# Performance work log

Hardware: AMD Instinct MI355X
Metric: run time of the kernel (lower is better)

## Reference

```python
import jax, jax.numpy as jnp
import numpy as np
import math

# ---- constants lifted verbatim from the torch source ----
PMLX = 10; PX = 400; TX = PMLX + PX + PMLX          # txsize = 420
PMLY = 10; PY = 400; TY = PMLY + PY + PMLY          # tysize = 420
CX = TX // 2; CY = TY // 2
EPS0 = 1e-9 / 36 / math.pi
MU0 = 4 * math.pi * 1e-7
C0 = 1.0 / math.sqrt(MU0 * EPS0)
DX = 2.5e-8; DY = 2.5e-8
DT = 0.99 / C0 / math.sqrt((1.0 / DX) ** 2 + (1.0 / DY) ** 2)
EPSR_INF = 5.283
EPS_INF = EPS0 * EPSR_INF
F0 = 5.47e14; BW = 0.1 * F0
T = math.sqrt(2.0) * math.sqrt(math.log(2.0)) / (math.pi * BW)
NSTEPS = 200   # reduced from 16000 for the correctness baseline; same per-step math


def setup_inputs() -> dict:
    # Lorentz (complex-pole) silver model from param(): pole/residue -> a0,a1,b0,b1,b2
    pr, pi_ = -4.8113e12, 6.8512e13
    rr, ri = 4.9581e14, -1.511e18
    a0 = -2.0 * (pr * rr + pi_ * ri)
    a1 = 2.0 * rr
    b0 = pr * pr + pi_ * pi_
    b1 = -2.0 * pr
    b2 = 1.0
    den = b0 * DT * DT + 2 * b1 * DT + 4 * b2
    Ca = np.array([-(2 * b0 * DT * DT - 8 * b2) / den], np.float32)
    Cb = np.array([-(b0 * DT * DT - 2 * b1 * DT + 4 * b2) / den], np.float32)
    Cc = np.array([(2 * a0 * EPS0 * DT + 4 * a1 * EPS0) / den], np.float32)
    Cd = np.array([-(8 * a1 * EPS0) / den], np.float32)
    Ce = np.array([(-2 * a0 * EPS0 * DT + 4 * a1 * EPS0) / den], np.float32)
    temp1 = float(Cc[0])                       # sum over tot_pol = 1 pole
    denom = EPS_INF / DT + 0.5 * temp1
    C1 = np.full((TX + 1, TY + 1), (EPS_INF / DT) / denom, np.float32)
    C2 = np.full((TX + 1, TY + 1), 0.5 / denom, np.float32)
    Cb_dx = np.full((TX + 1, TY + 1), 1.0 / denom / DX, np.float32)
    Cb_dy = np.full((TX + 1, TY + 1), 1.0 / denom / DY, np.float32)
    dbhx = np.full((TX + 1, TY), DT / MU0 / DY, np.float32)   # Hx curl coeff
    dbhy = np.full((TX, TY + 1), DT / MU0 / DX, np.float32)   # Hy curl coeff
    # polynomial-graded PML conductivity profiles (pml_param)
    m = 4
    eta0 = 120.0 * math.pi
    smax = 0.8 * (m + 1) / (eta0 * DX)

    def prof(n, npml, off):
        k = np.arange(n, dtype=np.float64)
        dl = np.clip(npml - k - off, 0.0, None) / npml   # depth into left PML
        dr = np.clip(k + off - (n - 1 - npml), 0.0, None) / npml
        return (smax * (dl ** m + dr ** m)).astype(np.float32)

    sig_ex = prof(TX + 1, PMLX, 0.0)
    sig_ey = prof(TY + 1, PMLY, 0.0)
    sig_hx = prof(TX, PMLX, 0.5)   # H nodes on half-grid
    sig_hy = prof(TY, PMLY, 0.5)
    # Gaussian-modulated sine soft source at the grid center
    t = np.arange(NSTEPS, dtype=np.float64) * DT
    src = (np.exp(-(((t - 4 * T) / T) ** 2)) * np.sin(2 * math.pi * F0 * (t - 4 * T))).astype(np.float32)
    return {
        "src": jnp.asarray(src), "C1": jnp.asarray(C1), "C2": jnp.asarray(C2),
        "Cb_dx": jnp.asarray(Cb_dx), "Cb_dy": jnp.asarray(Cb_dy),
        "dbhx": jnp.asarray(dbhx), "dbhy": jnp.asarray(dbhy),
        "Ca": jnp.asarray(Ca), "Cb": jnp.asarray(Cb), "Cc": jnp.asarray(Cc),
        "Cd": jnp.asarray(Cd), "Ce": jnp.asarray(Ce),
        "sig_ex": jnp.asarray(sig_ex), "sig_ey": jnp.asarray(sig_ey),
        "sig_hx": jnp.asarray(sig_hx), "sig_hy": jnp.asarray(sig_hy),
        "n_steps": NSTEPS,
    }


def reference(src, C1, C2, Cb_dx, Cb_dy, dbhx, dbhy, Ca, Cb, Cc, Cd, Ce,
              sig_ex, sig_ey, sig_hx, sig_hy, n_steps):
    # PML damping factors (exponential time-stepping of the conductive loss)
    de = jnp.exp(-(sig_ex[:, None] + sig_ey[None, :]) * (DT / EPS0))     # (421,421) for Ez
    dhx = jnp.exp(-(sig_ex[:, None] + sig_hy[None, :]) * (DT / MU0))     # (421,420) for Hx
    dhy = jnp.exp(-(sig_hx[:, None] + sig_ey[None, :]) * (DT / MU0))     # (420,421) for Hy
    # PEC outer boundary mask
    mask = jnp.pad(jnp.ones((TX - 1, TY - 1), de.dtype), ((1, 1), (1, 1)))
    ca = Ca[:, None, None]; cb = Cb[:, None, None]; cc = Cc[:, None, None]
    cd = Cd[:, None, None]; ce = Ce[:, None, None]

    def step(carry, s):
        Ez, Eold, Hx, Hy, Jz, Jold = carry
        # H-field Yee updates with PML damping
        Hx = dhx * (Hx - dbhx * (Ez[:, 1:] - Ez[:, :-1]))
        Hy = dhy * (Hy + dbhy * (Ez[1:, :] - Ez[:-1, :]))
        # curls onto Ez nodes (interior), zero-padded at PEC boundary
        curlHy = jnp.pad(Hy[1:, :] - Hy[:-1, :], ((1, 1), (0, 0)))       # (421,421)
        curlHx = jnp.pad(Hx[:, 1:] - Hx[:, :-1], ((0, 0), (1, 1)))       # (421,421)
        # Lorentz ADE dispersion source term (tot_pol summed; Cc*Ez^{n+1} folded into C1/C2/Cb_*)
        Phi = jnp.sum((ca + 1.0) * Jz + cb * Jold + cd * Ez[None] + ce * Eold[None], axis=0)
        Ez_new = mask * de * (C1 * Ez + Cb_dx * curlHy - Cb_dy * curlHx - C2 * Phi)
        Ez_new = Ez_new.at[CX, CY].add(s)                                 # soft point source
        # polarization current recurrence
        Jz_new = ca * Jz + cb * Jold + cc * Ez_new[None] + cd * Ez[None] + ce * Eold[None]
        return (Ez_new, Ez, Hx, Hy, Jz_new, Jz), None

    z = jnp.zeros((TX + 1, TY + 1), src.dtype)
    init = (z, z,
            jnp.zeros((TX + 1, TY), src.dtype),
            jnp.zeros((TX, TY + 1), src.dtype),
            jnp.zeros((1, TX + 1, TY + 1), src.dtype),
            jnp.zeros((1, TX + 1, TY + 1), src.dtype))
    (Ez, _, _, _, _, _), _ = jax.lax.scan(step, init, src[:n_steps])
    return Ez
```

## Files before the change

### kernel.cpp

```cpp
#include <hip/hip_runtime.h>
#include <math.h>

#define NXr 421
#define CXr 210
#define NSTEPS_C 200

#define Bt   16
#define Kt   8
#define EXT  32
#define LROWS (EXT + 2)
#define SPITCH 36
#define NBLK 27
#define NPHASE (NSTEPS_C / Kt)

#define PP   448
#define PAD  8
#define CP   (CXr + PAD)
#define FSZ  (PP * PP)

struct PParams {
    float *aEz, *aEo, *aJz, *aJo, *aHx, *aHy;
    float *bEz, *bEo, *bJz, *bJo, *bHx, *bHy;
    const float *dexP, *deyP, *aexP, *aeyP, *ahxP, *ahyP;
    const float *C1a, *C2a, *Cbdxa, *Cbdya;
    const float *Caa, *Cba, *Cca, *Cda, *Cea, *dbhxa, *dbhya;
    const float *src;
};

__global__ void init_kernel(const float* __restrict__ sig_ex,
                            const float* __restrict__ sig_ey,
                            const float* __restrict__ sig_hx,
                            const float* __restrict__ sig_hy,
                            float de_fac, float dh_fac,
                            float* __restrict__ zero_base, int n_zero,
                            float* __restrict__ dexP, float* __restrict__ deyP,
                            float* __restrict__ aexP, float* __restrict__ aeyP,
                            float* __restrict__ ahxP, float* __restrict__ ahyP)
{
    int t = blockIdx.x * blockDim.x + threadIdx.x;
    int stride = gridDim.x * blockDim.x;
    for (int k = t; k < n_zero; k += stride) zero_base[k] = 0.0f;
    if (t < PP) {
        int g = t - PAD;
        dexP[t] = (g >= 1 && g <= NXr - 2) ? expf(-sig_ex[g] * de_fac) : 0.0f;
        deyP[t] = (g >= 1 && g <= NXr - 2) ? expf(-sig_ey[g] * de_fac) : 0.0f;
        aexP[t] = (g >= 0 && g <  NXr)     ? expf(-sig_ex[g] * dh_fac) : 0.0f;
        aeyP[t] = (g >= 0 && g <  NXr)     ? expf(-sig_ey[g] * dh_fac) : 0.0f;
        ahxP[t] = (g >= 0 && g <  NXr - 1) ? expf(-sig_hx[g] * dh_fac) : 0.0f;
        ahyP[t] = (g >= 0 && g <  NXr - 1) ? expf(-sig_hy[g] * dh_fac) : 0.0f;
    }
}

__global__ __launch_bounds__(256)
void phase_kernel(PParams p, int t, int b0, float* __restrict__ out,
                  int writeOut)
{
    __shared__ __align__(16) float sEz[2][LROWS][SPITCH];

    const int tid = threadIdx.x;
    const int tj = tid & 15, ti = tid >> 4;
    const int li0 = 2 * ti, lj0 = 2 * tj;

    const int gx = (int)gridDim.x;
    int orig = (int)blockIdx.y * gx + (int)blockIdx.x;
    int nwg = gx * gx;
    int q = nwg >> 3, rr = nwg & 7;
    int xcd = orig & 7, k = orig >> 3;
    int nid = (xcd < rr ? xcd * (q + 1) : rr * (q + 1) + (xcd - rr) * q) + k;
    int bx = nid % gx, by = nid / gx;

    const int r0 = (bx + b0) * Bt + li0;
    const int c0 = (by + b0) * Bt + lj0;

    const float ca = p.Caa[0], cb = p.Cba[0], cc = p.Cca[0];
    const float cd = p.Cda[0], ce = p.Cea[0];
    const float ca1 = ca + 1.0f;
    const float C1 = p.C1a[0], C2 = p.C2a[0];
    const float cbdx = p.Cbdxa[0], cbdy = p.Cbdya[0];
    const float dbhx0 = p.dbhxa[0], dbhy0 = p.dbhya[0];

    float dHx[2][2], dHy[2][2], dE[2][2], dHyU[2], dHxL[2];
    float srcw[2][2];
#pragma unroll
    for (int a = 0; a < 2; ++a)
#pragma unroll
        for (int b = 0; b < 2; ++b) {
            dHx[a][b] = p.aexP[r0 + a] * p.ahyP[c0 + b];
            dHy[a][b] = p.ahxP[r0 + a] * p.aeyP[c0 + b];
            dE[a][b]  = p.dexP[r0 + a] * p.deyP[c0 + b];
            srcw[a][b] = ((r0 + a == CP) && (c0 + b == CP)) ? 1.0f : 0.0f;
        }
    {
        float ahxU = (r0 > 0) ? p.ahxP[r0 - 1] : 0.0f;
        float ahyL = (c0 > 0) ? p.ahyP[c0 - 1] : 0.0f;
        dHyU[0] = ahxU * p.aeyP[c0];
        dHyU[1] = ahxU * p.aeyP[c0 + 1];
        dHxL[0] = p.aexP[r0] * ahyL;
        dHxL[1] = p.aexP[r0 + 1] * ahyL;
    }

    const bool odd = (t & 1) != 0;
    const float* cEz = odd ? p.bEz : p.aEz;
    const float* cEo = odd ? p.bEo : p.aEo;
    const float* cJz = odd ? p.bJz : p.aJz;
    const float* cJo = odd ? p.bJo : p.aJo;
    const float* cHx = odd ? p.bHx : p.aHx;
    const float* cHy = odd ? p.bHy : p.aHy;
    float* nEz = odd ? p.aEz : p.bEz;
    float* nEo = odd ? p.aEo : p.bEo;
    float* nJz = odd ? p.aJz : p.bJz;
    float* nJo = odd ? p.aJo : p.bJo;
    float* nHx = odd ? p.aHx : p.bHx;
    float* nHy = odd ? p.aHy : p.bHy;

    {
        float* sp = &sEz[0][0][0];
        for (int z = tid; z < 2 * LROWS * SPITCH; z += 256) sp[z] = 0.0f;
    }

    float ez[2][2], eo[2][2], jz[2][2], jo[2][2], hx[2][2], hy[2][2];
#pragma unroll
    for (int a = 0; a < 2; ++a) {
        int g = (r0 + a) * PP + c0;
        float2 v;
        v = *(const float2*)&cEz[g]; ez[a][0] = v.x; ez[a][1] = v.y;
        v = *(const float2*)&cEo[g]; eo[a][0] = v.x; eo[a][1] = v.y;
        v = *(const float2*)&cJz[g]; jz[a][0] = v.x; jz[a][1] = v.y;
        v = *(const float2*)&cJo[g]; jo[a][0] = v.x; jo[a][1] = v.y;
        v = *(const float2*)&cHx[g]; hx[a][0] = v.x; hx[a][1] = v.y;
        v = *(const float2*)&cHy[g]; hy[a][0] = v.x; hy[a][1] = v.y;
    }
    float hyU[2], hxL[2];
    {
        float2 v = *(const float2*)&cHy[(r0 - 1) * PP + c0];
        hyU[0] = v.x; hyU[1] = v.y;
        hxL[0] = cHx[r0 * PP + c0 - 1];
        hxL[1] = cHx[(r0 + 1) * PP + c0 - 1];
    }

    const int n0 = t * Kt;
    float svl[Kt];
#pragma unroll
    for (int s = 0; s < Kt; ++s) svl[s] = p.src[n0 + s];

    __syncthreads();

    for (int s = 0; s < Kt; ++s) {
        float (*S)[SPITCH] = sEz[s & 1];
        *(float2*)&S[1 + li0][2 + lj0] = make_float2(ez[0][0], ez[0][1]);
        *(float2*)&S[2 + li0][2 + lj0] = make_float2(ez[1][0], ez[1][1]);

        hx[0][0] = dHx[0][0] * (hx[0][0] - dbhx0 * (ez[0][1] - ez[0][0]));
        hx[1][0] = dHx[1][0] * (hx[1][0] - dbhx0 * (ez[1][1] - ez[1][0]));
        hy[0][0] = dHy[0][0] * (hy[0][0] + dbhy0 * (ez[1][0] - ez[0][0]));
        hy[0][1] = dHy[0][1] * (hy[0][1] + dbhy0 * (ez[1][1] - ez[0][1]));

        __syncthreads();

        float eR0 = S[1 + li0][4 + lj0];
        float eR1 = S[2 + li0][4 + lj0];
        float2 eD = *(float2*)&S[3 + li0][2 + lj0];
        float2 eU = *(float2*)&S[li0][2 + lj0];
        float eL0 = S[1 + li0][1 + lj0];
        float eL1 = S[2 + li0][1 + lj0];

        hx[0][1] = dHx[0][1] * (hx[0][1] - dbhx0 * (eR0 - ez[0][1]));
        hx[1][1] = dHx[1][1] * (hx[1][1] - dbhx0 * (eR1 - ez[1][1]));
        hy[1][0] = dHy[1][0] * (hy[1][0] + dbhy0 * (eD.x - ez[1][0]));
        hy[1][1] = dHy[1][1] * (hy[1][1] + dbhy0 * (eD.y - ez[1][1]));

        hyU[0] = dHyU[0] * (hyU[0] + dbhy0 * (ez[0][0] - eU.x));
        hyU[1] = dHyU[1] * (hyU[1] + dbhy0 * (ez[0][1] - eU.y));
        hxL[0] = dHxL[0] * (hxL[0] - dbhx0 * (ez[0][0] - eL0));
        hxL[1] = dHxL[1] * (hxL[1] - dbhx0 * (ez[1][0] - eL1));

        float sv = svl[s];
        float cHyv[2][2], cHxv[2][2];
        cHyv[0][0] = hy[0][0] - hyU[0];   cHxv[0][0] = hx[0][0] - hxL[0];
        cHyv[0][1] = hy[0][1] - hyU[1];   cHxv[0][1] = hx[0][1] - hx[0][0];
        cHyv[1][0] = hy[1][0] - hy[0][0]; cHxv[1][0] = hx[1][0] - hxL[1];
        cHyv[1][1] = hy[1][1] - hy[0][1]; cHxv[1][1] = hx[1][1] - hx[1][0];

#pragma unroll
        for (int a = 0; a < 2; ++a)
#pragma unroll
            for (int b = 0; b < 2; ++b) {
                float e = ez[a][b], eold = eo[a][b];
                float j = jz[a][b], jold = jo[a][b];
                float phi = ca1 * j + cb * jold + cd * e + ce * eold;
                float en = dE[a][b] *
                    (C1 * e + cbdx * cHyv[a][b] - cbdy * cHxv[a][b] - C2 * phi);
                en = fmaf(srcw[a][b], sv, en);
                float jn = phi - j + cc * en;
                eo[a][b] = e;  ez[a][b] = en;
                jo[a][b] = j;  jz[a][b] = jn;
            }
    }

    if (ti >= 4 && ti < 12 && tj >= 4 && tj < 12) {
#pragma unroll
        for (int a = 0; a < 2; ++a) {
            int g = (r0 + a) * PP + c0;
            *(float2*)&nEz[g] = make_float2(ez[a][0], ez[a][1]);
            *(float2*)&nEo[g] = make_float2(eo[a][0], eo[a][1]);
            *(float2*)&nJz[g] = make_float2(jz[a][0], jz[a][1]);
            *(float2*)&nJo[g] = make_float2(jo[a][0], jo[a][1]);
            *(float2*)&nHx[g] = make_float2(hx[a][0], hx[a][1]);
            *(float2*)&nHy[g] = make_float2(hy[a][0], hy[a][1]);
        }
        if (writeOut) {
#pragma unroll
            for (int a = 0; a < 2; ++a)
#pragma unroll
                for (int b = 0; b < 2; ++b) {
                    int gi = r0 + a - PAD, gj = c0 + b - PAD;
                    if (gi < NXr && gj < NXr)
                        out[gi * NXr + gj] = ez[a][b];
                }
        }
    }
}

extern "C" void kernel_launch(void* const* d_in, const int* in_sizes, int n_in,
                              void* d_out, int out_size, void* d_ws, size_t ws_size,
                              hipStream_t stream)
{
    const float* src    = (const float*)d_in[0];
    const float* C1     = (const float*)d_in[1];
    const float* C2     = (const float*)d_in[2];
    const float* Cb_dx  = (const float*)d_in[3];
    const float* Cb_dy  = (const float*)d_in[4];
    const float* dbhx   = (const float*)d_in[5];
    const float* dbhy   = (const float*)d_in[6];
    const float* Ca     = (const float*)d_in[7];
    const float* Cb     = (const float*)d_in[8];
    const float* Cc     = (const float*)d_in[9];
    const float* Cd     = (const float*)d_in[10];
    const float* Ce     = (const float*)d_in[11];
    const float* sig_ex = (const float*)d_in[12];
    const float* sig_ey = (const float*)d_in[13];
    const float* sig_hx = (const float*)d_in[14];
    const float* sig_hy = (const float*)d_in[15];

    const double EPS0 = 1e-9 / 36.0 / M_PI;
    const double MU0  = 4.0 * M_PI * 1e-7;
    const double C0   = 1.0 / sqrt(MU0 * EPS0);
    const double DXd  = 2.5e-8, DYd = 2.5e-8;
    const double DT   = 0.99 / C0 / sqrt(1.0 / (DXd * DXd) + 1.0 / (DYd * DYd));
    const float de_fac = (float)(DT / EPS0);
    const float dh_fac = (float)(DT / MU0);

    float* base = (float*)d_ws;
    float* fields = base + PP;
    float* w = fields + 12 * (size_t)FSZ;
    float* dexP = w; w += PP;
    float* deyP = w; w += PP;
    float* aexP = w; w += PP;
    float* aeyP = w; w += PP;
    float* ahxP = w; w += PP;
    float* ahyP = w; w += PP;

    PParams p;
    p.aEz = fields + 0 * (size_t)FSZ;  p.aEo = fields + 1 * (size_t)FSZ;
    p.aJz = fields + 2 * (size_t)FSZ;  p.aJo = fields + 3 * (size_t)FSZ;
    p.aHx = fields + 4 * (size_t)FSZ;  p.aHy = fields + 5 * (size_t)FSZ;
    p.bEz = fields + 6 * (size_t)FSZ;  p.bEo = fields + 7 * (size_t)FSZ;
    p.bJz = fields + 8 * (size_t)FSZ;  p.bJo = fields + 9 * (size_t)FSZ;
    p.bHx = fields + 10 * (size_t)FSZ; p.bHy = fields + 11 * (size_t)FSZ;
    p.dexP = dexP; p.deyP = deyP; p.aexP = aexP; p.aeyP = aeyP;
    p.ahxP = ahxP; p.ahyP = ahyP;
    p.C1a = C1; p.C2a = C2; p.Cbdxa = Cb_dx; p.Cbdya = Cb_dy;
    p.Caa = Ca; p.Cba = Cb; p.Cca = Cc; p.Cda = Cd; p.Cea = Ce;
    p.dbhxa = dbhx; p.dbhya = dbhy;
    p.src = src;

    init_kernel<<<512, 256, 0, stream>>>(sig_ex, sig_ey, sig_hx, sig_hy,
                                         de_fac, dh_fac,
                                         base, PP + 12 * FSZ,
                                         dexP, deyP, aexP, aeyP, ahxP, ahyP);

    dim3 blk(256);
    for (int t = 0; t < NPHASE; ++t) {
        int R  = 8 * t + 11;
        int lo = CP - R, hi = CP + R;
        int b0 = (lo - (EXT - 1)) / 16; if (b0 < 0) b0 = 0;
        int b1 = hi / 16;               if (b1 > NBLK - 1) b1 = NBLK - 1;
        dim3 g(b1 - b0 + 1, b1 - b0 + 1);
        phase_kernel<<<g, blk, 0, stream>>>(p, t, b0, (float*)d_out,
                                            (t == NPHASE - 1) ? 1 : 0);
    }
}
```

Measured before the change: 256.6 us.

## Deepen temporal blocking to 10 steps per phase and precompute Ez/J terms before sync

```diff
diff --git a/kernel.cpp b/kernel.cpp
--- a/kernel.cpp
+++ b/kernel.cpp
@@ -5,16 +5,18 @@
 #define CXr 210
 #define NSTEPS_C 200
 
-#define Bt   16
-#define Kt   8
+#define Bt   12
+#define Kt   10
 #define EXT  32
 #define LROWS (EXT + 2)
 #define SPITCH 36
-#define NBLK 27
+#define NBLK 36
 #define NPHASE (NSTEPS_C / Kt)
-
-#define PP   448
-#define PAD  8
+#define OWN_T0 5
+#define OWN_T1 11
+
+#define PP   456
+#define PAD  10
 #define CP   (CXr + PAD)
 #define FSZ  (PP * PP)
 
@@ -155,6 +157,17 @@
         hy[0][0] = dHy[0][0] * (hy[0][0] + dbhy0 * (ez[1][0] - ez[0][0]));
         hy[0][1] = dHy[0][1] * (hy[0][1] + dbhy0 * (ez[1][1] - ez[0][1]));
 
+        float base[2][2], pj[2][2];
+#pragma unroll
+        for (int a = 0; a < 2; ++a)
+#pragma unroll
+            for (int b = 0; b < 2; ++b) {
+                float e = ez[a][b], j = jz[a][b];
+                float phi = ca1 * j + cb * jo[a][b] + cd * e + ce * eo[a][b];
+                base[a][b] = fmaf(-C2, phi, C1 * e);
+                pj[a][b] = phi - j;
+            }
+
         __syncthreads();
 
         float eR0 = S[1 + li0][4 + lj0];
@@ -185,19 +198,17 @@
         for (int a = 0; a < 2; ++a)
 #pragma unroll
             for (int b = 0; b < 2; ++b) {
-                float e = ez[a][b], eold = eo[a][b];
-                float j = jz[a][b], jold = jo[a][b];
-                float phi = ca1 * j + cb * jold + cd * e + ce * eold;
-                float en = dE[a][b] *
-                    (C1 * e + cbdx * cHyv[a][b] - cbdy * cHxv[a][b] - C2 * phi);
+                float v1 = fmaf(cbdx, cHyv[a][b], base[a][b]);
+                float v2 = fmaf(-cbdy, cHxv[a][b], v1);
+                float en = dE[a][b] * v2;
                 en = fmaf(srcw[a][b], sv, en);
-                float jn = phi - j + cc * en;
-                eo[a][b] = e;  ez[a][b] = en;
-                jo[a][b] = j;  jz[a][b] = jn;
+                float jn = fmaf(cc, en, pj[a][b]);
+                eo[a][b] = ez[a][b];  ez[a][b] = en;
+                jo[a][b] = jz[a][b];  jz[a][b] = jn;
             }
     }
 
-    if (ti >= 4 && ti < 12 && tj >= 4 && tj < 12) {
+    if (ti >= OWN_T0 && ti < OWN_T1 && tj >= OWN_T0 && tj < OWN_T1) {
 #pragma unroll
         for (int a = 0; a < 2; ++a) {
             int g = (r0 + a) * PP + c0;
@@ -281,10 +292,10 @@
 
     dim3 blk(256);
     for (int t = 0; t < NPHASE; ++t) {
-        int R  = 8 * t + 11;
+        int R  = 10 * t + 13;
         int lo = CP - R, hi = CP + R;
-        int b0 = (lo - (EXT - 1)) / 16; if (b0 < 0) b0 = 0;
-        int b1 = hi / 16;               if (b1 > NBLK - 1) b1 = NBLK - 1;
+        int b0 = (lo - (EXT - 1)) / Bt; if (b0 < 0) b0 = 0;
+        int b1 = hi / Bt;               if (b1 > NBLK - 1) b1 = NBLK - 1;
         dim3 g(b1 - b0 + 1, b1 - b0 + 1);
         phase_kernel<<<g, blk, 0, stream>>>(p, t, b0, (float*)d_out,
                                             (t == NPHASE - 1) ? 1 : 0);
```

After: 263.1 us. 2.6% more time.
